# Performance work log

Hardware: AMD Instinct MI355X
Metric: run time of the kernel (lower is better)

Reference implementation:

```python
import jax, jax.numpy as jnp
import numpy as np

N = 100_000   # nodes
E = 640_000   # edges
H = 128       # hidden_dim
L = 4         # num_layers
C = 2         # num_classes
G = 128       # graphs in batch

def setup_inputs() -> dict:
    key = jax.random.key(0)
    ks = jax.random.split(key, 8)
    x = jax.random.randint(ks[0], (N, 1), 0, 2)
    edge_index = jax.random.randint(ks[1], (2, E), 0, N)
    batch = jnp.sort(jax.random.randint(ks[2], (N,), 0, G))
    embed = jax.random.normal(ks[3], (2, H), jnp.float32)
    Ws = jax.random.normal(ks[4], (L, H, H), jnp.float32) * (1.0 / np.sqrt(H))
    bs = jnp.zeros((L, H), jnp.float32)
    W_out = jax.random.normal(ks[5], (H, C), jnp.float32) * (1.0 / np.sqrt(H))
    b_out = jnp.zeros((C,), jnp.float32)
    return dict(x=x, edge_index=edge_index, batch=batch, embed=embed,
                Ws=Ws, bs=bs, W_out=W_out, b_out=b_out)

def reference(x, edge_index, batch, embed, Ws, bs, W_out, b_out):
    src, dst = edge_index[0], edge_index[1]
    # symmetric GCN normalization with self-loops (PyG GCNConv default)
    deg = jax.ops.segment_sum(jnp.ones(E, jnp.float32), dst, num_segments=N) + 1.0
    dinv = jax.lax.rsqrt(deg)
    enorm = (dinv[src] * dinv[dst])[:, None]   # per-edge norm
    snorm = (dinv * dinv)[:, None]             # self-loop norm

    h = embed[x[:, 0]]                          # [N, H] embedding lookup
    n_layers = Ws.shape[0]
    for l in range(n_layers):
        t = h @ Ws[l]                           # linear transform [N, H]
        agg = jax.ops.segment_sum(t[src] * enorm, dst, num_segments=N) \
              + t * snorm + bs[l]
        h = jax.nn.relu(agg) if l < n_layers - 1 else agg

    # global mean pool over graph ids
    counts = jax.ops.segment_sum(jnp.ones(N, jnp.float32), batch, num_segments=G)
    pooled = jax.ops.segment_sum(h, batch, num_segments=G) \
             / jnp.maximum(counts, 1.0)[:, None]   # [G, H]
    return pooled @ W_out + b_out                  # [G, C]
```

## Files before the change

### kernel.cpp

```cpp
#include <hip/hip_runtime.h>

typedef __attribute__((ext_vector_type(8))) short bf16x8;
typedef __attribute__((ext_vector_type(4))) float f32x4;
typedef __attribute__((ext_vector_type(2))) float f32x2;

__device__ inline unsigned short bf16_rtn(float f) {
  unsigned u = __float_as_uint(f);
  unsigned r = u + 0x7fffu + ((u >> 16) & 1u);
  return (unsigned short)(r >> 16);
}

__device__ inline void split_bf16(float f, unsigned short& hi, unsigned short& lo) {
  hi = bf16_rtn(f);
  float fh = __uint_as_float((unsigned)hi << 16);
  lo = bf16_rtn(f - fh);
}

__device__ inline float bf16_to_f(unsigned short v) {
  return __uint_as_float((unsigned)v << 16);
}

__device__ inline unsigned char f_to_fp8(float f) {
  int r = __builtin_amdgcn_cvt_pk_fp8_f32(f, f, 0, false);
  return (unsigned char)(r & 0xff);
}
__device__ inline f32x2 fp8x2_to_f(unsigned short v) {
  return __builtin_amdgcn_cvt_pk_f32_fp8((int)v, false);
}

__global__ void k_init(int* __restrict__ deg, int* __restrict__ gpz, int N, int M,
                       const float* __restrict__ Ws, const float* __restrict__ embed,
                       unsigned short* __restrict__ wphi,
                       unsigned short* __restrict__ wplo,
                       float* __restrict__ T,
                       unsigned char* __restrict__ t_a,
                       unsigned char* __restrict__ t_b) {
  int i = blockIdx.x * 256 + threadIdx.x;
  if (i < N) deg[i] = 0;
  if (i < M) gpz[i] = 0;
  int l = blockIdx.x;
  if (l < 3) {
    const float* W = Ws + (size_t)(l + 1) * 128 * 128;
    unsigned short* dh = wphi + (size_t)l * 16384;
    unsigned short* dl = wplo + (size_t)l * 16384;
    for (int idx = threadIdx.x; idx < 16384; idx += 256) {
      int j = idx & 7;
      int lane = (idx >> 3) & 63;
      int c = (idx >> 9) & 3;
      int ct = idx >> 11;
      int k = c * 32 + ((lane >> 4) * 8) + j;
      int n = ct * 16 + (lane & 15);
      unsigned short hi, lo;
      split_bf16(W[k * 128 + n], hi, lo);
      dh[idx] = hi;
      dl[idx] = lo;
    }
  } else if (l == 3) {
    int t = threadIdx.x;
    int r = t >> 7, c = t & 127;
    float acc = 0.f;
    for (int k = 0; k < 128; ++k)
      acc += embed[r * 128 + k] * Ws[k * 128 + c];
    T[r * 128 + c] = acc;
  } else if (l == 4) {
    int t = threadIdx.x;
    if (t < 32)      ((unsigned*)(t_a + (size_t)N * 128))[t] = 0u;
    else if (t < 64) ((unsigned*)(t_b + (size_t)N * 128))[t - 32] = 0u;
  }
}


__global__ void k_hist(const int* __restrict__ dst, int* __restrict__ deg,
                       int* __restrict__ posr, int E) {
  int e = blockIdx.x * 256 + threadIdx.x;
  if (e < E) posr[e] = atomicAdd(&deg[dst[e]], 1);
}

__global__ void k_scan1(const int* __restrict__ deg, int* __restrict__ rowptr,
                        int* __restrict__ bsum, float* __restrict__ dpk,
                        const int* __restrict__ x, const int* __restrict__ batch,
                        int* __restrict__ gstart, int* __restrict__ gend, int N) {
  __shared__ int s[256];
  int t = threadIdx.x;
  int i = blockIdx.x * 256 + t;
  int v = (i < N) ? deg[i] : 0;
  if (i < N) {
    float di = rsqrtf((float)v + 1.0f);
    dpk[i] = x[i] ? -di : di;
    int g = batch[i];
    if (i == 0 || batch[i - 1] != g) gstart[g] = i;
    if (i == N - 1 || batch[i + 1] != g) gend[g] = i + 1;
  }
  s[t] = v;
  __syncthreads();
  for (int off = 1; off < 256; off <<= 1) {
    int u = (t >= off) ? s[t - off] : 0;
    __syncthreads();
    s[t] += u;
    __syncthreads();
  }
  if (i < N) rowptr[i] = s[t] - v;
  if (t == 255) bsum[blockIdx.x] = s[255];
}

__global__ void k_scan2(const int* __restrict__ bsum, int* __restrict__ boff, int nb) {
  __shared__ int s[512];
  int t = threadIdx.x;
  int v = (t < nb) ? bsum[t] : 0;
  s[t] = v;
  __syncthreads();
  for (int off = 1; off < 512; off <<= 1) {
    int u = (t >= off) ? s[t - off] : 0;
    __syncthreads();
    s[t] += u;
    __syncthreads();
  }
  boff[t] = s[t] - v;
}

__global__ void k_scan3(int* __restrict__ rowptr, const int* __restrict__ boff,
                        int N, int E) {
  int i = blockIdx.x * 256 + threadIdx.x;
  if (i < N) rowptr[i] += boff[i >> 8];
  if (i == 0) rowptr[N] = E;
}

__global__ void k_scatter(const int* __restrict__ src, const int* __restrict__ dst,
                          const int* __restrict__ posr, const int* __restrict__ rowptr,
                          const float* __restrict__ dpk,
                          int2* __restrict__ epack, int* __restrict__ esrc, int E) {
  int e = blockIdx.x * 256 + threadIdx.x;
  if (e >= E) return;
  int s = src[e], d = dst[e];
  int pos = rowptr[d] + posr[e];
  epack[pos] = make_int2(s, __float_as_int(dpk[s]));
  esrc[pos] = s;
}


__device__ inline void acc16(float* a, uint4 p) {
  f32x2 v;
  v = __builtin_amdgcn_cvt_pk_f32_fp8((int)p.x, false); a[0]  += v.x; a[1]  += v.y;
  v = __builtin_amdgcn_cvt_pk_f32_fp8((int)p.x, true);  a[2]  += v.x; a[3]  += v.y;
  v = __builtin_amdgcn_cvt_pk_f32_fp8((int)p.y, false); a[4]  += v.x; a[5]  += v.y;
  v = __builtin_amdgcn_cvt_pk_f32_fp8((int)p.y, true);  a[6]  += v.x; a[7]  += v.y;
  v = __builtin_amdgcn_cvt_pk_f32_fp8((int)p.z, false); a[8]  += v.x; a[9]  += v.y;
  v = __builtin_amdgcn_cvt_pk_f32_fp8((int)p.z, true);  a[10] += v.x; a[11] += v.y;
  v = __builtin_amdgcn_cvt_pk_f32_fp8((int)p.w, false); a[12] += v.x; a[13] += v.y;
  v = __builtin_amdgcn_cvt_pk_f32_fp8((int)p.w, true);  a[14] += v.x; a[15] += v.y;
}

__device__ inline void gather8(const unsigned char* __restrict__ tin,
                               const int* __restrict__ esrc,
                               int r0, int deg, int l8, int N,
                               float* a) {
  int dcap = deg < 16 ? deg : 16;
  int slo = N, shi = N;
  if (2 * l8 < dcap)     slo = esrc[r0 + 2 * l8];
  if (2 * l8 + 1 < dcap) shi = esrc[r0 + 2 * l8 + 1];

  uint4 p[16];
  #pragma unroll
  for (int k = 0; k < 8; ++k) {
    int se = __shfl(slo, k, 8);
    int so = __shfl(shi, k, 8);
    p[2 * k]     = *(const uint4*)(tin + (size_t)((unsigned)se * 128u + ((unsigned)l8 << 4)));
    p[2 * k + 1] = *(const uint4*)(tin + (size_t)((unsigned)so * 128u + ((unsigned)l8 << 4)));
  }
  #pragma unroll
  for (int k = 0; k < 16; ++k) acc16(a, p[k]);

  if (__builtin_expect(deg > 16, 0)) {
    for (int e = r0 + 16; e < r0 + deg; ++e) {
      int s = esrc[e];
      uint4 q = *(const uint4*)(tin + (size_t)((unsigned)s * 128u + ((unsigned)l8 << 4)));
      acc16(a, q);
    }
  }
}

__global__ __launch_bounds__(64)
void k_agg(const unsigned char* __restrict__ tin,
           const int* __restrict__ rowptr,
           const int* __restrict__ esrc,
           const float* __restrict__ dpk, const float* __restrict__ bvec,
           unsigned short* __restrict__ h, int N) {
  int lane = threadIdx.x;
  int g8 = lane >> 3, l8 = lane & 7;
  int i = blockIdx.x * 8 + g8;
  if (i >= N) return;
  int r0 = rowptr[i], r1 = rowptr[i + 1];
  uint4 ps = *(const uint4*)(tin + (size_t)i * 128 + (l8 << 4));
  float dp = dpk[i];

  float a[16];
  #pragma unroll
  for (int k = 0; k < 16; ++k) a[k] = 0.f;
  gather8(tin, esrc, r0, r1 - r0, l8, N, a);
  acc16(a, ps);

  float di = fabsf(dp);
  const float4* bp = (const float4*)(bvec + 16 * l8);
  float4 b0 = bp[0], b1 = bp[1], b2 = bp[2], b3 = bp[3];
  float bb[16] = {b0.x, b0.y, b0.z, b0.w, b1.x, b1.y, b1.z, b1.w,
                  b2.x, b2.y, b2.z, b2.w, b3.x, b3.y, b3.z, b3.w};
  unsigned u[8];
  #pragma unroll
  for (int k = 0; k < 8; ++k) {
    float v0 = fmaxf(di * a[2 * k]     + bb[2 * k],     0.f);
    float v1 = fmaxf(di * a[2 * k + 1] + bb[2 * k + 1], 0.f);
    u[k] = (unsigned)bf16_rtn(v0) | ((unsigned)bf16_rtn(v1) << 16);
  }
  uint4* hp = (uint4*)(h + (size_t)i * 128 + 16 * l8);
  hp[0] = make_uint4(u[0], u[1], u[2], u[3]);
  hp[1] = make_uint4(u[4], u[5], u[6], u[7]);
}

__global__ __launch_bounds__(64)
void k_agg_pool(const unsigned char* __restrict__ tin,
                const int* __restrict__ rowptr,
                const int* __restrict__ esrc,
                const float* __restrict__ dpk, const float* __restrict__ bvec,
                const int* __restrict__ batch,
                float* __restrict__ pooled, int N) {
  __shared__ float sh[8][128];
  __shared__ int sg[8];
  int lane = threadIdx.x;
  int g8 = lane >> 3, l8 = lane & 7;
  int i = blockIdx.x * 8 + g8;
  if (lane < 8) sg[lane] = -1;
  __syncthreads();
  if (i < N) {
    int r0 = rowptr[i], r1 = rowptr[i + 1];
    uint4 ps = *(const uint4*)(tin + (size_t)i * 128 + (l8 << 4));
    float dp = dpk[i];

    float a[16];
    #pragma unroll
    for (int k = 0; k < 16; ++k) a[k] = 0.f;
    gather8(tin, esrc, r0, r1 - r0, l8, N, a);
    acc16(a, ps);

    float di = fabsf(dp);
    const float4* bp = (const float4*)(bvec + 16 * l8);
    float4 b0 = bp[0], b1 = bp[1], b2 = bp[2], b3 = bp[3];
    float bb[16] = {b0.x, b0.y, b0.z, b0.w, b1.x, b1.y, b1.z, b1.w,
                    b2.x, b2.y, b2.z, b2.w, b3.x, b3.y, b3.z, b3.w};
    #pragma unroll
    for (int k = 0; k < 16; ++k)
      sh[g8][16 * l8 + k] = di * a[k] + bb[k];
    if (l8 == 0) sg[g8] = batch[i];
  }
  __syncthreads();
  #pragma unroll
  for (int cc = 0; cc < 2; ++cc) {
    int c = threadIdx.x + 64 * cc;
    float acc = 0.f;
    int cur = sg[0];
    #pragma unroll
    for (int w2 = 0; w2 < 8; ++w2) {
      int gw = sg[w2];
      if (gw < 0) break;
      if (gw != cur) {
        atomicAdd(&pooled[cur * 128 + c], acc);
        acc = 0.f;
        cur = gw;
      }
      acc += sh[w2][c];
    }
    if (cur >= 0) atomicAdd(&pooled[cur * 128 + c], acc);
  }
}

__global__ void k_gemm(const unsigned short* __restrict__ h,
                       const unsigned short* __restrict__ wphi,
                       const unsigned short* __restrict__ wplo,
                       const float* __restrict__ dpk,
                       unsigned char* __restrict__ tout, int N) {
  int wave = threadIdx.x >> 6;
  int lane = threadIdx.x & 63;
  int r0 = (blockIdx.x * 4 + wave) * 32;
  if (r0 >= N) return;
  int q = lane >> 4;
  int m = lane & 15;
  const bf16x8* bh_base = (const bf16x8*)wphi;
  const bf16x8* bl_base = (const bf16x8*)wplo;

  f32x4 acc[2][8];
  #pragma unroll
  for (int tt = 0; tt < 2; ++tt)
    #pragma unroll
    for (int ct = 0; ct < 8; ++ct)
      acc[tt][ct] = (f32x4){0.f, 0.f, 0.f, 0.f};

  for (int c = 0; c < 4; ++c) {
    bf16x8 a0 = *(const bf16x8*)(h + (size_t)(r0 + m) * 128 + c * 32 + q * 8);
    bf16x8 a1 = *(const bf16x8*)(h + (size_t)(r0 + 16 + m) * 128 + c * 32 + q * 8);
    #pragma unroll
    for (int ct = 0; ct < 8; ++ct) {
      bf16x8 bh = bh_base[(ct * 4 + c) * 64 + lane];
      bf16x8 bl = bl_base[(ct * 4 + c) * 64 + lane];
      acc[0][ct] = __builtin_amdgcn_mfma_f32_16x16x32_bf16(a0, bh, acc[0][ct], 0, 0, 0);
      acc[0][ct] = __builtin_amdgcn_mfma_f32_16x16x32_bf16(a0, bl, acc[0][ct], 0, 0, 0);
      acc[1][ct] = __builtin_amdgcn_mfma_f32_16x16x32_bf16(a1, bh, acc[1][ct], 0, 0, 0);
      acc[1][ct] = __builtin_amdgcn_mfma_f32_16x16x32_bf16(a1, bl, acc[1][ct], 0, 0, 0);
    }
  }

  #pragma unroll
  for (int tt = 0; tt < 2; ++tt)
    #pragma unroll
    for (int ct = 0; ct < 8; ++ct)
      #pragma unroll
      for (int r = 0; r < 4; ++r) {
        int row = r0 + tt * 16 + q * 4 + r;
        if (row < N) {
          float sc = fabsf(dpk[row]);
          tout[(size_t)row * 128 + ct * 16 + m] = f_to_fp8(sc * acc[tt][ct][r]);
        }
      }
}

__device__ inline void gemm_tile8(const unsigned short* hT,
                                  const unsigned short* __restrict__ wphi,
                                  const unsigned short* __restrict__ wplo,
                                  const float* __restrict__ dpk,
                                  unsigned char* __restrict__ tout, int i0, int N) {
  int ct = threadIdx.x >> 6;
  int lane = threadIdx.x & 63;
  int q = lane >> 4;
  int m = lane & 15;
  const bf16x8* bh_base = (const bf16x8*)wphi;
  const bf16x8* bl_base = (const bf16x8*)wplo;

  f32x4 acc0 = (f32x4){0.f, 0.f, 0.f, 0.f};
  f32x4 acc1 = (f32x4){0.f, 0.f, 0.f, 0.f};

  #pragma unroll
  for (int c = 0; c < 4; ++c) {
    bf16x8 a0 = *(const bf16x8*)(hT + (m) * 136 + c * 32 + q * 8);
    bf16x8 a1 = *(const bf16x8*)(hT + (16 + m) * 136 + c * 32 + q * 8);
    bf16x8 bh = bh_base[(ct * 4 + c) * 64 + lane];
    bf16x8 bl = bl_base[(ct * 4 + c) * 64 + lane];
    acc0 = __builtin_amdgcn_mfma_f32_16x16x32_bf16(a0, bh, acc0, 0, 0, 0);
    acc0 = __builtin_amdgcn_mfma_f32_16x16x32_bf16(a0, bl, acc0, 0, 0, 0);
    acc1 = __builtin_amdgcn_mfma_f32_16x16x32_bf16(a1, bh, acc1, 0, 0, 0);
    acc1 = __builtin_amdgcn_mfma_f32_16x16x32_bf16(a1, bl, acc1, 0, 0, 0);
  }

  #pragma unroll
  for (int r = 0; r < 4; ++r) {
    int row0 = i0 + q * 4 + r;
    int row1 = row0 + 16;
    if (row0 < N) {
      float sc = fabsf(dpk[row0]);
      tout[(size_t)row0 * 128 + ct * 16 + m] = f_to_fp8(sc * acc0[r]);
    }
    if (row1 < N) {
      float sc = fabsf(dpk[row1]);
      tout[(size_t)row1 * 128 + ct * 16 + m] = f_to_fp8(sc * acc1[r]);
    }
  }
}

__global__ __launch_bounds__(512)
void k_l1_gemm(const int* __restrict__ rowptr,
               const int2* __restrict__ epack,
               const float* __restrict__ dpk, const float* __restrict__ T,
               const float* __restrict__ b0,
               const unsigned short* __restrict__ wphi,
               const unsigned short* __restrict__ wplo,
               unsigned char* __restrict__ tout, int N) {
  __shared__ unsigned short hT[32 * 136];
  int wave = threadIdx.x >> 6;
  int lane = threadIdx.x & 63;
  int i0 = blockIdx.x * 32;

  for (int j = wave * 4; j < wave * 4 + 4; ++j) {
    int i = i0 + j;
    if (i >= N) break;
    int r0 = rowptr[i], r1 = rowptr[i + 1];
    float sabs = 0.f, sneg = 0.f;
    for (int e = r0 + lane; e < r1; e += 64) {
      float wv = __int_as_float(epack[e].y);
      float aw = fabsf(wv);
      sabs += aw;
      if (wv < 0.f) sneg += aw;
    }
    for (int mm = 32; mm >= 1; mm >>= 1) {
      sabs += __shfl_xor(sabs, mm, 64);
      sneg += __shfl_xor(sneg, mm, 64);
    }
    float dp = dpk[i];
    float di = fabsf(dp);
    float sn = di * di;
    float c1 = di * sneg;
    float c0 = di * (sabs - sneg);
    if (dp < 0.f) c1 += sn; else c0 += sn;
    float v0 = fmaxf(c0 * T[2 * lane]     + c1 * T[128 + 2 * lane]     + b0[2 * lane],     0.f);
    float v1 = fmaxf(c0 * T[2 * lane + 1] + c1 * T[128 + 2 * lane + 1] + b0[2 * lane + 1], 0.f);
    *(unsigned*)&hT[j * 136 + 2 * lane] = (unsigned)bf16_rtn(v0) | ((unsigned)bf16_rtn(v1) << 16);
  }
  __syncthreads();
  gemm_tile8(hT, wphi, wplo, dpk, tout, i0, N);
}

__global__ void k_out(const float* __restrict__ pooled, const int* __restrict__ gstart,
                      const int* __restrict__ gend, const float* __restrict__ W_out,
                      const float* __restrict__ b_out, float* __restrict__ out, int G) {
  __shared__ float sp[128];
  int g = blockIdx.x;
  int j = threadIdx.x;
  float cnt = (float)(gend[g] - gstart[g]);
  sp[j] = pooled[g * 128 + j] / fmaxf(cnt, 1.f);
  __syncthreads();
  if (j < 2) {
    float o = b_out[j];
    for (int k = 0; k < 128; ++k)
      o += sp[k] * W_out[k * 2 + j];
    out[g * 2 + j] = o;
  }
}

extern "C" void kernel_launch(void* const* d_in, const int* in_sizes, int n_in,
                              void* d_out, int out_size, void* d_ws, size_t ws_size,
                              hipStream_t stream) {
  const int*   x     = (const int*)d_in[0];
  const int*   ei    = (const int*)d_in[1];
  const int*   batch = (const int*)d_in[2];
  const float* embed = (const float*)d_in[3];
  const float* Ws    = (const float*)d_in[4];
  const float* bs    = (const float*)d_in[5];
  const float* W_out = (const float*)d_in[6];
  const float* b_out = (const float*)d_in[7];
  float* out = (float*)d_out;

  int N = in_sizes[2];
  int E = in_sizes[1] / 2;
  int G = out_size / 2;

  const int* src = ei;
  const int* dst = ei + E;

  char* w = (char*)d_ws;
  auto alloc = [&](size_t bytes) {
    char* p = w;
    w += (bytes + 255) & ~(size_t)255;
    return p;
  };
  int*   deg    = (int*)  alloc((size_t)N * 4);
  float* dpk    = (float*)alloc((size_t)N * 4);
  int*   rowptr = (int*)  alloc((size_t)(N + 1) * 4);
  int*   posr   = (int*)  alloc((size_t)E * 4);
  int*   bsum   = (int*)  alloc(512 * 4);
  int*   boff   = (int*)  alloc(512 * 4);
  int*   gstart = (int*)  alloc((size_t)G * 4);
  int*   gend   = (int*)  alloc((size_t)G * 4);
  float* pooled = (float*)alloc((size_t)G * 128 * 4);
  float* T      = (float*)alloc(256 * 4);
  unsigned short* wphi = (unsigned short*)alloc((size_t)3 * 16384 * 2);
  unsigned short* wplo = (unsigned short*)alloc((size_t)3 * 16384 * 2);
  int2*  epack  = (int2*) alloc((size_t)E * 8);
  int*   esrc   = (int*)  alloc((size_t)E * 4);
  unsigned short* h = (unsigned short*)alloc((size_t)N * 128 * 2);
  unsigned char* t_a = (unsigned char*)alloc((size_t)(N + 1) * 128);
  unsigned char* t_b = (unsigned char*)alloc((size_t)(N + 1) * 128);

  int nbN = (N + 255) / 256;
  int nbE = (E + 255) / 256;
  int ntile = (N + 31) / 32;
  int nagg = (N + 7) / 8;
  int ngemm = (N + 127) / 128;
  int M = G * 130;

  k_init<<<nbN, 256, 0, stream>>>(deg, gstart, N, M, Ws, embed, wphi, wplo, T, t_a, t_b);
  k_hist<<<nbE, 256, 0, stream>>>(dst, deg, posr, E);
  k_scan1<<<nbN, 256, 0, stream>>>(deg, rowptr, bsum, dpk, x, batch, gstart, gend, N);
  k_scan2<<<1, 512, 0, stream>>>(bsum, boff, nbN);
  k_scan3<<<nbN, 256, 0, stream>>>(rowptr, boff, N, E);
  k_scatter<<<nbE, 256, 0, stream>>>(src, dst, posr, rowptr, dpk, epack, esrc, E);

  k_l1_gemm<<<ntile, 512, 0, stream>>>(rowptr, epack, dpk, T, bs,
                                       wphi, wplo, t_a, N);
  k_agg<<<nagg, 64, 0, stream>>>(t_a, rowptr, esrc, dpk, bs + 128, h, N);
  k_gemm<<<ngemm, 256, 0, stream>>>(h, wphi + 16384, wplo + 16384, dpk, t_b, N);
  k_agg<<<nagg, 64, 0, stream>>>(t_b, rowptr, esrc, dpk, bs + 256, h, N);
  k_gemm<<<ngemm, 256, 0, stream>>>(h, wphi + 32768, wplo + 32768, dpk, t_a, N);
  k_agg_pool<<<nagg, 64, 0, stream>>>(t_a, rowptr, esrc, dpk, bs + 384,
                                      batch, pooled, N);
  k_out<<<G, 128, 0, stream>>>(pooled, gstart, gend, W_out, b_out, out, G);
}
```

Measured before the change: 294.5 us.

## Store fp8 features in column-slice-major layout and aggregate per slice

The GEMM outputs now write the fp8 transformed features as 8 column slices of 16 bytes per node, each slice contiguous across nodes. Aggregation kernels give one thread per node per slice, with blockIdx encoding the slice. Each thread gathers 16-byte rows from a slice table that is 1/8 the size, which is meant to improve L2 locality of the random neighbor gathers. In exchange, each edge index is read 8 times (once per slice), and the pool kernel's atomic reduction over nodes changes shape.

```diff
diff --git a/kernel.cpp b/kernel.cpp
--- a/kernel.cpp
+++ b/kernel.cpp
@@ -16,16 +16,21 @@
   lo = bf16_rtn(f - fh);
 }
 
-__device__ inline float bf16_to_f(unsigned short v) {
-  return __uint_as_float((unsigned)v << 16);
-}
-
 __device__ inline unsigned char f_to_fp8(float f) {
   int r = __builtin_amdgcn_cvt_pk_fp8_f32(f, f, 0, false);
   return (unsigned char)(r & 0xff);
 }
-__device__ inline f32x2 fp8x2_to_f(unsigned short v) {
-  return __builtin_amdgcn_cvt_pk_f32_fp8((int)v, false);
+
+__device__ inline void acc16(float* a, uint4 p) {
+  f32x2 v;
+  v = __builtin_amdgcn_cvt_pk_f32_fp8((int)p.x, false); a[0]  += v.x; a[1]  += v.y;
+  v = __builtin_amdgcn_cvt_pk_f32_fp8((int)p.x, true);  a[2]  += v.x; a[3]  += v.y;
+  v = __builtin_amdgcn_cvt_pk_f32_fp8((int)p.y, false); a[4]  += v.x; a[5]  += v.y;
+  v = __builtin_amdgcn_cvt_pk_f32_fp8((int)p.y, true);  a[6]  += v.x; a[7]  += v.y;
+  v = __builtin_amdgcn_cvt_pk_f32_fp8((int)p.z, false); a[8]  += v.x; a[9]  += v.y;
+  v = __builtin_amdgcn_cvt_pk_f32_fp8((int)p.z, true);  a[10] += v.x; a[11] += v.y;
+  v = __builtin_amdgcn_cvt_pk_f32_fp8((int)p.w, false); a[12] += v.x; a[13] += v.y;
+  v = __builtin_amdgcn_cvt_pk_f32_fp8((int)p.w, true);  a[14] += v.x; a[15] += v.y;
 }
 
 __global__ void k_init(int* __restrict__ deg, int* __restrict__ gpz, int N, int M,
@@ -64,11 +69,15 @@
     T[r * 128 + c] = acc;
   } else if (l == 4) {
     int t = threadIdx.x;
-    if (t < 32)      ((unsigned*)(t_a + (size_t)N * 128))[t] = 0u;
-    else if (t < 64) ((unsigned*)(t_b + (size_t)N * 128))[t - 32] = 0u;
-  }
-}
-
+    if (t < 32) {
+      int s = t >> 2, wd = t & 3;
+      ((unsigned*)(t_a + ((size_t)s * (N + 1) + N) * 16))[wd] = 0u;
+    } else if (t < 64) {
+      int t2 = t - 32, s = t2 >> 2, wd = t2 & 3;
+      ((unsigned*)(t_b + ((size_t)s * (N + 1) + N) * 16))[wd] = 0u;
+    }
+  }
+}
 
 __global__ void k_hist(const int* __restrict__ dst, int* __restrict__ deg,
                        int* __restrict__ posr, int E) {
@@ -138,72 +147,52 @@
 }
 
 
-__device__ inline void acc16(float* a, uint4 p) {
-  f32x2 v;
-  v = __builtin_amdgcn_cvt_pk_f32_fp8((int)p.x, false); a[0]  += v.x; a[1]  += v.y;
-  v = __builtin_amdgcn_cvt_pk_f32_fp8((int)p.x, true);  a[2]  += v.x; a[3]  += v.y;
-  v = __builtin_amdgcn_cvt_pk_f32_fp8((int)p.y, false); a[4]  += v.x; a[5]  += v.y;
-  v = __builtin_amdgcn_cvt_pk_f32_fp8((int)p.y, true);  a[6]  += v.x; a[7]  += v.y;
-  v = __builtin_amdgcn_cvt_pk_f32_fp8((int)p.z, false); a[8]  += v.x; a[9]  += v.y;
-  v = __builtin_amdgcn_cvt_pk_f32_fp8((int)p.z, true);  a[10] += v.x; a[11] += v.y;
-  v = __builtin_amdgcn_cvt_pk_f32_fp8((int)p.w, false); a[12] += v.x; a[13] += v.y;
-  v = __builtin_amdgcn_cvt_pk_f32_fp8((int)p.w, true);  a[14] += v.x; a[15] += v.y;
-}
-
-__device__ inline void gather8(const unsigned char* __restrict__ tin,
-                               const int* __restrict__ esrc,
-                               int r0, int deg, int l8, int N,
-                               float* a) {
-  int dcap = deg < 16 ? deg : 16;
-  int slo = N, shi = N;
-  if (2 * l8 < dcap)     slo = esrc[r0 + 2 * l8];
-  if (2 * l8 + 1 < dcap) shi = esrc[r0 + 2 * l8 + 1];
-
-  uint4 p[16];
-  #pragma unroll
-  for (int k = 0; k < 8; ++k) {
-    int se = __shfl(slo, k, 8);
-    int so = __shfl(shi, k, 8);
-    p[2 * k]     = *(const uint4*)(tin + (size_t)((unsigned)se * 128u + ((unsigned)l8 << 4)));
-    p[2 * k + 1] = *(const uint4*)(tin + (size_t)((unsigned)so * 128u + ((unsigned)l8 << 4)));
-  }
-  #pragma unroll
-  for (int k = 0; k < 16; ++k) acc16(a, p[k]);
-
+__device__ inline void gather_sl(const unsigned char* __restrict__ ts,
+                                 const int* __restrict__ esrc,
+                                 int i, int r0, int deg, int N, float* a) {
+  int idx[16];
+  #pragma unroll
+  for (int e = 0; e < 16; ++e) {
+    int ie = esrc[r0 + e];
+    idx[e] = (e < deg) ? ie : N;
+  }
+  uint4 p[17];
+  #pragma unroll
+  for (int e = 0; e < 16; ++e)
+    p[e] = *(const uint4*)(ts + (size_t)idx[e] * 16);
+  p[16] = *(const uint4*)(ts + (size_t)i * 16);
+  #pragma unroll
+  for (int e = 0; e < 17; ++e) acc16(a, p[e]);
   if (__builtin_expect(deg > 16, 0)) {
     for (int e = r0 + 16; e < r0 + deg; ++e) {
-      int s = esrc[e];
-      uint4 q = *(const uint4*)(tin + (size_t)((unsigned)s * 128u + ((unsigned)l8 << 4)));
+      uint4 q = *(const uint4*)(ts + (size_t)esrc[e] * 16);
       acc16(a, q);
     }
   }
 }
 
-__global__ __launch_bounds__(64)
-void k_agg(const unsigned char* __restrict__ tin,
-           const int* __restrict__ rowptr,
-           const int* __restrict__ esrc,
-           const float* __restrict__ dpk, const float* __restrict__ bvec,
-           unsigned short* __restrict__ h, int N) {
-  int lane = threadIdx.x;
-  int g8 = lane >> 3, l8 = lane & 7;
-  int i = blockIdx.x * 8 + g8;
+__global__ __launch_bounds__(256)
+void k_agg_sl(const unsigned char* __restrict__ tin,
+              const int* __restrict__ rowptr,
+              const int* __restrict__ esrc,
+              const float* __restrict__ dpk, const float* __restrict__ bvec,
+              unsigned short* __restrict__ h, int N) {
+  int slice = blockIdx.x & 7;
+  int i = (blockIdx.x >> 3) * 256 + threadIdx.x;
   if (i >= N) return;
+  const unsigned char* ts = tin + (size_t)slice * (N + 1) * 16;
   int r0 = rowptr[i], r1 = rowptr[i + 1];
-  uint4 ps = *(const uint4*)(tin + (size_t)i * 128 + (l8 << 4));
-  float dp = dpk[i];
-
-  float a[16];
-  #pragma unroll
-  for (int k = 0; k < 16; ++k) a[k] = 0.f;
-  gather8(tin, esrc, r0, r1 - r0, l8, N, a);
-  acc16(a, ps);
-
-  float di = fabsf(dp);
-  const float4* bp = (const float4*)(bvec + 16 * l8);
+  float di = fabsf(dpk[i]);
+  const float4* bp = (const float4*)(bvec + slice * 16);
   float4 b0 = bp[0], b1 = bp[1], b2 = bp[2], b3 = bp[3];
   float bb[16] = {b0.x, b0.y, b0.z, b0.w, b1.x, b1.y, b1.z, b1.w,
                   b2.x, b2.y, b2.z, b2.w, b3.x, b3.y, b3.z, b3.w};
+
+  float a[16];
+  #pragma unroll
+  for (int k = 0; k < 16; ++k) a[k] = 0.f;
+  gather_sl(ts, esrc, i, r0, r1 - r0, N, a);
+
   unsigned u[8];
   #pragma unroll
   for (int k = 0; k < 8; ++k) {
@@ -211,65 +200,58 @@
     float v1 = fmaxf(di * a[2 * k + 1] + bb[2 * k + 1], 0.f);
     u[k] = (unsigned)bf16_rtn(v0) | ((unsigned)bf16_rtn(v1) << 16);
   }
-  uint4* hp = (uint4*)(h + (size_t)i * 128 + 16 * l8);
+  uint4* hp = (uint4*)(h + (size_t)i * 128 + slice * 16);
   hp[0] = make_uint4(u[0], u[1], u[2], u[3]);
   hp[1] = make_uint4(u[4], u[5], u[6], u[7]);
 }
 
-__global__ __launch_bounds__(64)
-void k_agg_pool(const unsigned char* __restrict__ tin,
-                const int* __restrict__ rowptr,
-                const int* __restrict__ esrc,
-                const float* __restrict__ dpk, const float* __restrict__ bvec,
-                const int* __restrict__ batch,
-                float* __restrict__ pooled, int N) {
-  __shared__ float sh[8][128];
-  __shared__ int sg[8];
-  int lane = threadIdx.x;
-  int g8 = lane >> 3, l8 = lane & 7;
-  int i = blockIdx.x * 8 + g8;
-  if (lane < 8) sg[lane] = -1;
-  __syncthreads();
+__global__ __launch_bounds__(256)
+void k_agg_pool_sl(const unsigned char* __restrict__ tin,
+                   const int* __restrict__ rowptr,
+                   const int* __restrict__ esrc,
+                   const float* __restrict__ dpk, const float* __restrict__ bvec,
+                   const int* __restrict__ batch,
+                   float* __restrict__ pooled, int N) {
+  __shared__ float sh[256][16];
+  __shared__ int sg[256];
+  int slice = blockIdx.x & 7;
+  int i = (blockIdx.x >> 3) * 256 + threadIdx.x;
+  sg[threadIdx.x] = -1;
   if (i < N) {
+    const unsigned char* ts = tin + (size_t)slice * (N + 1) * 16;
     int r0 = rowptr[i], r1 = rowptr[i + 1];
-    uint4 ps = *(const uint4*)(tin + (size_t)i * 128 + (l8 << 4));
-    float dp = dpk[i];
-
+    float di = fabsf(dpk[i]);
+    const float4* bp = (const float4*)(bvec + slice * 16);
+    float4 b0 = bp[0], b1 = bp[1], b2 = bp[2], b3 = bp[3];
+    float bb[16] = {b0.x, b0.y, b0.z, b0.w, b1.x, b1.y, b1.z, b1.w,
+                    b2.x, b2.y, b2.z, b2.w, b3.x, b3.y, b3.z, b3.w};
     float a[16];
     #pragma unroll
     for (int k = 0; k < 16; ++k) a[k] = 0.f;
-    gather8(tin, esrc, r0, r1 - r0, l8, N, a);
-    acc16(a, ps);
-
-    float di = fabsf(dp);
-    const float4* bp = (const float4*)(bvec + 16 * l8);
-    float4 b0 = bp[0], b1 = bp[1], b2 = bp[2], b3 = bp[3];
-    float bb[16] = {b0.x, b0.y, b0.z, b0.w, b1.x, b1.y, b1.z, b1.w,
-                    b2.x, b2.y, b2.z, b2.w, b3.x, b3.y, b3.z, b3.w};
+    gather_sl(ts, esrc, i, r0, r1 - r0, N, a);
     #pragma unroll
     for (int k = 0; k < 16; ++k)
-      sh[g8][16 * l8 + k] = di * a[k] + bb[k];
-    if (l8 == 0) sg[g8] = batch[i];
+      sh[threadIdx.x][k] = di * a[k] + bb[k];
+    sg[threadIdx.x] = batch[i];
   }
   __syncthreads();
-  #pragma unroll
-  for (int cc = 0; cc < 2; ++cc) {
-    int c = threadIdx.x + 64 * cc;
-    float acc = 0.f;
-    int cur = sg[0];
-    #pragma unroll
-    for (int w2 = 0; w2 < 8; ++w2) {
-      int gw = sg[w2];
-      if (gw < 0) break;
-      if (gw != cur) {
-        atomicAdd(&pooled[cur * 128 + c], acc);
-        acc = 0.f;
-        cur = gw;
-      }
-      acc += sh[w2][c];
-    }
-    if (cur >= 0) atomicAdd(&pooled[cur * 128 + c], acc);
-  }
+  int c = threadIdx.x & 15;
+  int k = threadIdx.x >> 4;
+  int base = k * 16;
+  float acc = 0.f;
+  int cur = sg[base];
+  #pragma unroll
+  for (int j = 0; j < 16; ++j) {
+    int g = sg[base + j];
+    if (g < 0) break;
+    if (g != cur) {
+      atomicAdd(&pooled[cur * 128 + slice * 16 + c], acc);
+      acc = 0.f;
+      cur = g;
+    }
+    acc += sh[base + j][c];
+  }
+  if (cur >= 0) atomicAdd(&pooled[cur * 128 + slice * 16 + c], acc);
 }
 
 __global__ void k_gemm(const unsigned short* __restrict__ h,
@@ -316,7 +298,8 @@
         int row = r0 + tt * 16 + q * 4 + r;
         if (row < N) {
           float sc = fabsf(dpk[row]);
-          tout[(size_t)row * 128 + ct * 16 + m] = f_to_fp8(sc * acc[tt][ct][r]);
+          tout[(size_t)ct * ((size_t)(N + 1) * 16) + (size_t)row * 16 + m] =
+              f_to_fp8(sc * acc[tt][ct][r]);
         }
       }
 }
@@ -348,17 +331,18 @@
     acc1 = __builtin_amdgcn_mfma_f32_16x16x32_bf16(a1, bl, acc1, 0, 0, 0);
   }
 
+  size_t sbase = (size_t)ct * ((size_t)(N + 1) * 16);
   #pragma unroll
   for (int r = 0; r < 4; ++r) {
     int row0 = i0 + q * 4 + r;
     int row1 = row0 + 16;
     if (row0 < N) {
       float sc = fabsf(dpk[row0]);
-      tout[(size_t)row0 * 128 + ct * 16 + m] = f_to_fp8(sc * acc0[r]);
+      tout[sbase + (size_t)row0 * 16 + m] = f_to_fp8(sc * acc0[r]);
     }
     if (row1 < N) {
       float sc = fabsf(dpk[row1]);
-      tout[(size_t)row1 * 128 + ct * 16 + m] = f_to_fp8(sc * acc1[r]);
+      tout[sbase + (size_t)row1 * 16 + m] = f_to_fp8(sc * acc1[r]);
     }
   }
 }
@@ -461,7 +445,7 @@
   unsigned short* wphi = (unsigned short*)alloc((size_t)3 * 16384 * 2);
   unsigned short* wplo = (unsigned short*)alloc((size_t)3 * 16384 * 2);
   int2*  epack  = (int2*) alloc((size_t)E * 8);
-  int*   esrc   = (int*)  alloc((size_t)E * 4);
+  int*   esrc   = (int*)  alloc((size_t)(E + 16) * 4);
   unsigned short* h = (unsigned short*)alloc((size_t)N * 128 * 2);
   unsigned char* t_a = (unsigned char*)alloc((size_t)(N + 1) * 128);
   unsigned char* t_b = (unsigned char*)alloc((size_t)(N + 1) * 128);
@@ -469,8 +453,8 @@
   int nbN = (N + 255) / 256;
   int nbE = (E + 255) / 256;
   int ntile = (N + 31) / 32;
-  int nagg = (N + 7) / 8;
   int ngemm = (N + 127) / 128;
+  int nsl = ((N + 255) / 256) * 8;
   int M = G * 130;
 
   k_init<<<nbN, 256, 0, stream>>>(deg, gstart, N, M, Ws, embed, wphi, wplo, T, t_a, t_b);
@@ -482,11 +466,11 @@
 
   k_l1_gemm<<<ntile, 512, 0, stream>>>(rowptr, epack, dpk, T, bs,
                                        wphi, wplo, t_a, N);
-  k_agg<<<nagg, 64, 0, stream>>>(t_a, rowptr, esrc, dpk, bs + 128, h, N);
+  k_agg_sl<<<nsl, 256, 0, stream>>>(t_a, rowptr, esrc, dpk, bs + 128, h, N);
   k_gemm<<<ngemm, 256, 0, stream>>>(h, wphi + 16384, wplo + 16384, dpk, t_b, N);
-  k_agg<<<nagg, 64, 0, stream>>>(t_b, rowptr, esrc, dpk, bs + 256, h, N);
+  k_agg_sl<<<nsl, 256, 0, stream>>>(t_b, rowptr, esrc, dpk, bs + 256, h, N);
   k_gemm<<<ngemm, 256, 0, stream>>>(h, wphi + 32768, wplo + 32768, dpk, t_a, N);
-  k_agg_pool<<<nagg, 64, 0, stream>>>(t_a, rowptr, esrc, dpk, bs + 384,
-                                      batch, pooled, N);
+  k_agg_pool_sl<<<nsl, 256, 0, stream>>>(t_a, rowptr, esrc, dpk, bs + 384,
+                                         batch, pooled, N);
   k_out<<<G, 128, 0, stream>>>(pooled, gstart, gend, W_out, b_out, out, G);
 }
```

New measurement: 333.5 us. 13.2% more time.
